# Kernel optimization log

Hardware: AMD Instinct MI355X
Metric: run time of the kernel (lower is better)

Reference implementation:

```python
import jax, jax.numpy as jnp
import numpy as np

NHEAD = 4
EPS_RMS = 1e-6
EPS_LN = 1e-5
KEEP_RATE = 0.7


def _adj_diag(num_joints=25):
    # NTU parent-child pairs; note torch.einsum('sjj,sntjc->sntjc', adj, x)
    # takes the DIAGONAL of each adjacency -> only adj_root (identity) survives,
    # adj_close/adj_far have zero diagonals. We reproduce that math faithfully.
    pairs = [(20, 1), (1, 0), (20, 2), (2, 3), (20, 4), (4, 5), (5, 6), (6, 7),
             (7, 21), (7, 22), (20, 8), (8, 9), (9, 10), (10, 11), (11, 23),
             (11, 24), (0, 12), (12, 13), (13, 14), (14, 15), (0, 16), (16, 17),
             (17, 18), (18, 19)]
    root = np.eye(num_joints, dtype=np.float32)
    close = np.zeros((num_joints, num_joints), dtype=np.float32)
    far = np.zeros((num_joints, num_joints), dtype=np.float32)
    for p, c in pairs:
        close[p, c] = 1.0
        far[c, p] = 1.0
    adj = np.stack([root, close, far])  # [3, J, J]
    return jnp.asarray(np.stack([np.diag(a) for a in adj]))  # [3, J]


def rmsnorm(x, w):
    return x * jax.lax.rsqrt(jnp.mean(x * x, -1, keepdims=True) + EPS_RMS) * w


def layernorm(x, w, b):
    m = jnp.mean(x, -1, keepdims=True)
    v = jnp.mean((x - m) ** 2, -1, keepdims=True)
    return (x - m) * jax.lax.rsqrt(v + EPS_LN) * w + b


def mha(x, in_w, in_b, out_w, out_b):
    # torch nn.MultiheadAttention (batch_first, eval: dropout off)
    B, L, C = x.shape
    H = NHEAD
    hd = C // H
    qkv = x @ in_w.T + in_b  # [B, L, 3C]
    q, k, v = jnp.split(qkv, 3, axis=-1)
    heads = lambda t: t.reshape(B, L, H, hd).transpose(0, 2, 1, 3)
    q, k, v = heads(q), heads(k), heads(v)
    attn = jax.nn.softmax(jnp.einsum('bhqd,bhkd->bhqk', q, k) / np.sqrt(hd).astype(np.float32), -1)
    o = jnp.einsum('bhqk,bhkd->bhqd', attn, v).transpose(0, 2, 1, 3).reshape(B, L, C)
    return o @ out_w.T + out_b, attn  # attn: [B, H, L, L] (average_attn_weights=False)


def reference(x, prev_spatial_attn_scores, gcn_w, g_norm_w, cls_tok, sn1_w, sn2_w,
              s_in_w, s_in_b, s_out_w, s_out_b, s_f1w, s_f1b, s_f2w, s_f2b,
              t_in_w, t_in_b, t_out_w, t_out_b, t_ln1w, t_ln1b, t_ln2w, t_ln2b,
              t_f1w, t_f1b, t_f2w, t_f2b, tn_w):
    N, T, J, _ = x.shape
    C = gcn_w.shape[-1]
    NT = N * T
    k = int(J * KEEP_RATE)
    diag = _adj_diag(J)  # [3, J]

    res = x  # residual = Identity (in_features == out_features)
    # ShiftGraphConvolution (diagonal einsum semantics) + RMSNorm
    x_gcn = rmsnorm(jnp.einsum('sj,ntjc,scd->ntjd', diag, x, gcn_w), g_norm_w)
    res_spatial = x_gcn
    xs = x_gcn.reshape(NT, J, C)

    # top-k token selection from previous cls-attention scores
    order = jnp.argsort(-prev_spatial_attn_scores, axis=1)  # descending
    idx_keep = order[:, :k]  # [NT, k]
    idx_drop = order[:, k:]  # [NT, J-k]
    ph_scores = jnp.take_along_axis(prev_spatial_attn_scores, idx_drop, 1)
    ph_norm = jax.nn.softmax(ph_scores, 1)[..., None]  # [NT, J-k, 1]
    x_inf = jnp.take_along_axis(xs, idx_keep[..., None], 1)  # [NT, k, C]
    x_ph = jnp.take_along_axis(xs, idx_drop[..., None], 1)   # [NT, J-k, C]
    x_rep = jnp.sum(x_ph * ph_norm, 1, keepdims=True)        # [NT, 1, C]

    cls = jnp.broadcast_to(cls_tok, (NT, 1, C))
    x_slow = jnp.concatenate([cls, x_inf, x_rep], 1)  # [NT, k+2, C]

    attn_out, attn_w = mha(rmsnorm(x_slow, sn1_w), s_in_w, s_in_b, s_out_w, s_out_b)
    x_msa = x_slow + attn_out
    ffn = jax.nn.gelu(rmsnorm(x_msa, sn2_w) @ s_f1w.T + s_f1b, approximate=False) @ s_f2w.T + s_f2b
    x_final_slow = x_msa + ffn

    # next spatial attention scores (cls -> other tokens, head-averaged)
    cls2others = attn_w[:, :, 0, 1:].mean(1)  # [NT, k+1]
    batch = jnp.arange(NT)[:, None]
    next_attn = jnp.zeros((NT, J), x.dtype)
    next_attn = next_attn.at[batch, idx_keep].set(cls2others[:, :k])
    next_attn = next_attn.at[batch, idx_drop].set(jnp.broadcast_to(cls2others[:, k:], (NT, J - k)))

    # scatter kept + placeholder tokens back to joint positions
    x_rep_res = attn_out[:, 1 + k:, :] + ffn[:, 1 + k:, :]  # [NT, 1, C]
    x_ph_out = x_ph + jnp.broadcast_to(x_rep_res, (NT, J - k, C))
    x_inf_out = x_final_slow[:, 1:1 + k, :]
    x_sp = jnp.zeros_like(xs)
    x_sp = x_sp.at[batch, idx_keep].set(x_inf_out)
    x_sp = x_sp.at[batch, idx_drop].set(x_ph_out)
    x_sp = x_sp.reshape(N, T, J, C) + res_spatial

    # temporal TransformerEncoderLayer (post-norm, gelu) + RMSNorm
    xt = x_sp.transpose(0, 2, 1, 3).reshape(N * J, T, C)
    a, _ = mha(xt, t_in_w, t_in_b, t_out_w, t_out_b)
    xt = layernorm(xt + a, t_ln1w, t_ln1b)
    f = jax.nn.gelu(xt @ t_f1w.T + t_f1b, approximate=False) @ t_f2w.T + t_f2b
    xt = layernorm(xt + f, t_ln2w, t_ln2b)
    xt = rmsnorm(xt, tn_w)
    x_t = xt.reshape(N, J, T, C).transpose(0, 2, 1, 3) + x_sp
    return x_t + res, next_attn


def setup_inputs() -> dict:
    key = jax.random.key(0)
    N, T, J, C, DFF = 64, 120, 25, 128, 256
    ks = jax.random.split(key, 16)
    g = lambda k_, shp: (jax.random.normal(k_, shp, jnp.float32) * 0.02)
    return {
        'x': jax.random.normal(ks[0], (N, T, J, C), jnp.float32),
        'prev_spatial_attn_scores': jax.random.uniform(ks[1], (N * T, J), jnp.float32),
        'gcn_w': g(ks[2], (3, C, C)),
        'g_norm_w': jnp.ones((C,), jnp.float32),
        'cls_tok': jnp.zeros((1, 1, C), jnp.float32),
        'sn1_w': jnp.ones((C,), jnp.float32),
        'sn2_w': jnp.ones((C,), jnp.float32),
        's_in_w': g(ks[3], (3 * C, C)), 's_in_b': jnp.zeros((3 * C,), jnp.float32),
        's_out_w': g(ks[4], (C, C)), 's_out_b': jnp.zeros((C,), jnp.float32),
        's_f1w': g(ks[5], (DFF, C)), 's_f1b': jnp.zeros((DFF,), jnp.float32),
        's_f2w': g(ks[6], (C, DFF)), 's_f2b': jnp.zeros((C,), jnp.float32),
        't_in_w': g(ks[7], (3 * C, C)), 't_in_b': jnp.zeros((3 * C,), jnp.float32),
        't_out_w': g(ks[8], (C, C)), 't_out_b': jnp.zeros((C,), jnp.float32),
        't_ln1w': jnp.ones((C,), jnp.float32), 't_ln1b': jnp.zeros((C,), jnp.float32),
        't_ln2w': jnp.ones((C,), jnp.float32), 't_ln2b': jnp.zeros((C,), jnp.float32),
        't_f1w': g(ks[9], (DFF, C)), 't_f1b': jnp.zeros((DFF,), jnp.float32),
        't_f2w': g(ks[10], (C, DFF)), 't_f2b': jnp.zeros((C,), jnp.float32),
        'tn_w': jnp.ones((C,), jnp.float32),
    }
```

## Files before the change

### kernel.cpp

```cpp
#include <hip/hip_runtime.h>
#include <hip/hip_bf16.h>
#include <math.h>

#define NTR   7680
#define NJ    25
#define NKEEP 17
#define NDRP  8
#define NL    19
#define NROW  192000
#define NTT   120
#define RSP   24

typedef __attribute__((ext_vector_type(8))) short bf16x8;
typedef __attribute__((ext_vector_type(4))) float f32x4;

__device__ __forceinline__ float gelu_exact(float v){
    return 0.5f * v * (1.0f + erff(v * 0.70710678118654752440f));
}
__device__ __forceinline__ unsigned short f2bf(float v){
    union { __hip_bfloat16 h; unsigned short u; } c;
    c.h = __float2bfloat16(v);
    return c.u;
}
__device__ __forceinline__ float bf2f(unsigned short u){
    union { unsigned u; float f; } a; a.u = ((unsigned)u) << 16; return a.f;
}

__global__ void k_prep(const float* __restrict__ s_in_w, const float* __restrict__ s_out_w,
                       const float* __restrict__ s_f1w,  const float* __restrict__ s_f2w,
                       const float* __restrict__ t_in_w, const float* __restrict__ t_out_w,
                       const float* __restrict__ t_f1w,  const float* __restrict__ t_f2w,
                       const float* __restrict__ gcnw,
                       const float* __restrict__ sn1w,   const float* __restrict__ sn2w,
                       unsigned short* __restrict__ WM)
{
    int i = blockIdx.x * 256 + threadIdx.x;
    if (i < 65536){
        const float* src;
        const float* nw = nullptr;
        int base;
        if      (i < 12288){ src = s_in_w;  base = 0;     nw = sn1w; }
        else if (i < 16384){ src = s_out_w; base = 12288; }
        else if (i < 24576){ src = s_f1w;   base = 16384; nw = sn2w; }
        else if (i < 32768){ src = s_f2w;   base = 24576; }
        else if (i < 45056){ src = t_in_w;  base = 32768; }
        else if (i < 49152){ src = t_out_w; base = 45056; }
        else if (i < 57344){ src = t_f1w;   base = 49152; }
        else               { src = t_f2w;   base = 57344; }
        int loc = i - base;
        float4 v = *(const float4*)(src + loc * 4);
        if (nw){
            float4 w = *(const float4*)(nw + ((loc * 4) & 127));
            v.x *= w.x; v.y *= w.y; v.z *= w.z; v.w *= w.w;
        }
        ushort4 o; o.x = f2bf(v.x); o.y = f2bf(v.y); o.z = f2bf(v.z); o.w = f2bf(v.w);
        *(ushort4*)(WM + i * 4) = o;
    } else if (i < 81920){
        int j = i - 65536;
        int d = j >> 7, c = j & 127;
        WM[262144 + d * 128 + c] = f2bf(gcnw[c * 128 + d]);
    }
}

__global__ __launch_bounds__(256, 3) void k_gcn_mfma(
    const float* __restrict__ x, const unsigned short* __restrict__ GWt,
    const float* __restrict__ gnw, unsigned short* __restrict__ xg)
{
    __shared__ __align__(16) unsigned short xb[64 * 136];
    __shared__ __align__(16) float yf[64 * 132];
    __shared__ float ssq[64];
    __shared__ float rstd[64];
    int tid = threadIdx.x, wv = tid >> 6, lane = tid & 63, cl = lane & 15, g = lane >> 4;
    size_t row0 = (size_t)blockIdx.x * 64;

    if (tid < 64) ssq[tid] = 0.f;
    const float4* x4 = (const float4*)(x + row0 * 128);
    for (int i = tid; i < 2048; i += 256){
        int row = i >> 5, ch = i & 31;
        float4 v = x4[row * 32 + ch];
        ushort4 o; o.x = f2bf(v.x); o.y = f2bf(v.y); o.z = f2bf(v.z); o.w = f2bf(v.w);
        *(ushort4*)(xb + row * 136 + ch * 4) = o;
    }
    __syncthreads();
    for (int job = wv; job < 32; job += 4){
        int rt = job >> 3, ct = job & 7, col = ct * 16 + cl;
        f32x4 acc = {0.f, 0.f, 0.f, 0.f};
        #pragma unroll
        for (int ks = 0; ks < 4; ks++){
            bf16x8 a = *(const bf16x8*)(xb + (rt*16 + cl)*136 + ks*32 + g*8);
            bf16x8 b = *(const bf16x8*)(GWt + col*128 + ks*32 + g*8);
            acc = __builtin_amdgcn_mfma_f32_16x16x32_bf16(a, b, acc, 0, 0, 0);
        }
        #pragma unroll
        for (int reg = 0; reg < 4; reg++){
            int row = rt*16 + g*4 + reg;
            float v = acc[reg];
            yf[row*132 + col] = v;
            float p = v * v;
            p += __shfl_xor(p, 1, 64); p += __shfl_xor(p, 2, 64);
            p += __shfl_xor(p, 4, 64); p += __shfl_xor(p, 8, 64);
            if (cl == 0) atomicAdd(&ssq[row], p);
        }
    }
    __syncthreads();
    if (tid < 64) rstd[tid] = rsqrtf(ssq[tid] * 0.0078125f + 1e-6f);
    __syncthreads();
    for (int i = tid; i < 2048; i += 256){
        int row = i >> 5, ch = i & 31;
        float4 v = *(const float4*)(yf + row*132 + ch*4);
        float4 w4 = *(const float4*)(gnw + ch*4);
        float r = rstd[row];
        ushort4 u;
        u.x = f2bf(v.x * r * w4.x); u.y = f2bf(v.y * r * w4.y);
        u.z = f2bf(v.z * r * w4.z); u.w = f2bf(v.w * r * w4.w);
        *(ushort4*)(xg + (row0 + row)*128 + ch*4) = u;
    }
}

__global__ void k_select(const float* __restrict__ sc, int* __restrict__ order,
                         int* __restrict__ slot, float* __restrict__ ph){
    int r = blockIdx.x * blockDim.x + threadIdx.x;
    if (r >= NTR) return;
    float s[NJ]; int id[NJ];
    for (int j = 0; j < NJ; j++){ s[j] = sc[r * NJ + j]; id[j] = j; }
    for (int m = 1; m < NJ; m++){
        float sv = s[m]; int iv = id[m]; int p = m;
        while (p > 0 && s[p-1] < sv){ s[p] = s[p-1]; id[p] = id[p-1]; p--; }
        s[p] = sv; id[p] = iv;
    }
    for (int j = 0; j < NJ; j++) order[r * NJ + j] = id[j];
    for (int i = 0; i < NKEEP; i++)  slot[r * NJ + id[i]] = 1 + i;
    for (int i = NKEEP; i < NJ; i++) slot[r * NJ + id[i]] = 18;
    float m8 = s[NKEEP];
    float e[NDRP]; float sum = 0.f;
    for (int i = 0; i < NDRP; i++){ e[i] = expf(s[NKEEP + i] - m8); sum += e[i]; }
    float inv = 1.f / sum;
    for (int i = 0; i < NDRP; i++) ph[r * NDRP + i] = e[i] * inv;
}

__global__ __launch_bounds__(512, 4) void k_spatial8(
    const unsigned short* __restrict__ xg, const int* __restrict__ order, const float* __restrict__ ph,
    const float* __restrict__ cls_tok,
    const unsigned short* __restrict__ WinB, const float* __restrict__ inb,
    const unsigned short* __restrict__ WoutB, const float* __restrict__ outb,
    const unsigned short* __restrict__ F1B, const float* __restrict__ f1b,
    const unsigned short* __restrict__ F2B, const float* __restrict__ f2b,
    unsigned short* __restrict__ delta, float* __restrict__ next_attn)
{
    __shared__ __align__(16) unsigned short sm[39680];
    __shared__ float rstd[48];
    __shared__ float ss2[48];
    __shared__ float clsp[8][20];
    __shared__ int   ord_s[2][NJ];
    __shared__ float ph_s[2][NDRP];
    unsigned short* xs = sm;
    unsigned short* Pb = sm + 6528;
    unsigned short* qk = sm + 16768;
    unsigned short* vT = sm + 29440;
    unsigned short* ao = sm + 29440;

    int tid = threadIdx.x;
    int r0 = blockIdx.x * 2;
    int wv = tid >> 6, lane = tid & 63, cl = lane & 15, g = lane >> 4;
    const float scale = 0.17677669529663687f;

    if (tid < 2*NJ)   ord_s[tid/NJ][tid%NJ] = order[(r0 + tid/NJ)*NJ + tid%NJ];
    if (tid < 2*NDRP) ph_s[tid>>3][tid&7]   = ph[(r0 + (tid>>3))*NDRP + (tid&7)];
    if (tid < 48) ss2[tid] = 0.f;
    for (int i = tid; i < 1280; i += 512)
        *(uint4*)(vT + i*8) = make_uint4(0,0,0,0);
    __syncthreads();

    {
        int ln = tid & 31;
        for (int j = tid >> 5; j < 48; j += 16){
            int rr = j / RSP, t = j - rr * RSP;
            const unsigned short* xgr = xg + (size_t)(r0 + rr) * NJ * 128;
            float v0, v1, v2, v3;
            if (t == 0){
                float4 cv = *(const float4*)(cls_tok + ln*4);
                v0 = cv.x; v1 = cv.y; v2 = cv.z; v3 = cv.w;
            } else if (t <= NKEEP){
                ushort4 u = *(const ushort4*)(xgr + ord_s[rr][t-1]*128 + ln*4);
                v0 = bf2f(u.x); v1 = bf2f(u.y); v2 = bf2f(u.z); v3 = bf2f(u.w);
            } else if (t == 18){
                v0 = v1 = v2 = v3 = 0.f;
                for (int i = 0; i < NDRP; i++){
                    ushort4 u = *(const ushort4*)(xgr + ord_s[rr][NKEEP+i]*128 + ln*4);
                    float w = ph_s[rr][i];
                    v0 = fmaf(bf2f(u.x),w,v0); v1 = fmaf(bf2f(u.y),w,v1);
                    v2 = fmaf(bf2f(u.z),w,v2); v3 = fmaf(bf2f(u.w),w,v3);
                }
            } else { v0 = v1 = v2 = v3 = 0.f; }
            ushort4 o4; o4.x=f2bf(v0); o4.y=f2bf(v1); o4.z=f2bf(v2); o4.w=f2bf(v3);
            *(ushort4*)(xs + j*136 + ln*4) = o4;
            float p = v0*v0 + v1*v1 + v2*v2 + v3*v3;
            p += __shfl_xor(p, 1, 64); p += __shfl_xor(p, 2, 64);
            p += __shfl_xor(p, 4, 64); p += __shfl_xor(p, 8, 64);
            p += __shfl_xor(p, 16, 64);
            if (ln == 0) rstd[j] = rsqrtf(p * 0.0078125f + 1e-6f);
        }
    }
    __syncthreads();

    {
        int col = wv*16 + cl;
        bf16x8 Bq[4], Bk[4], Bv[4];
        #pragma unroll
        for (int ks = 0; ks < 4; ks++){
            Bq[ks] = *(const bf16x8*)(WinB + col*128        + ks*32 + g*8);
            Bk[ks] = *(const bf16x8*)(WinB + (128+col)*128  + ks*32 + g*8);
            Bv[ks] = *(const bf16x8*)(WinB + (256+col)*128  + ks*32 + g*8);
        }
        float bq = inb[col], bk = inb[128+col], bv = inb[256+col];
        int h = col >> 5, d = col & 31;
        #pragma unroll
        for (int rt = 0; rt < 3; rt++){
            bf16x8 A[4];
            #pragma unroll
            for (int ks = 0; ks < 4; ks++)
                A[ks] = *(const bf16x8*)(xs + (rt*16 + cl)*136 + ks*32 + g*8);
            f32x4 aq = {0,0,0,0}, ak = {0,0,0,0}, av = {0,0,0,0};
            #pragma unroll
            for (int ks = 0; ks < 4; ks++){
                aq = __builtin_amdgcn_mfma_f32_16x16x32_bf16(A[ks], Bq[ks], aq, 0, 0, 0);
                ak = __builtin_amdgcn_mfma_f32_16x16x32_bf16(A[ks], Bk[ks], ak, 0, 0, 0);
                av = __builtin_amdgcn_mfma_f32_16x16x32_bf16(A[ks], Bv[ks], av, 0, 0, 0);
            }
            #pragma unroll
            for (int reg = 0; reg < 4; reg++){
                int row = rt*16 + g*4 + reg;
                float rs = rstd[row];
                qk[row*264 + col]       = f2bf((aq[reg]*rs + bq) * scale);
                qk[row*264 + 128 + col] = f2bf(ak[reg]*rs + bk);
                int rr = row >= RSP; int key = row - rr*RSP;
                vT[(rr*4 + h)*1280 + d*40 + key] = f2bf(av[reg]*rs + bv);
            }
        }
    }
    __syncthreads();

    {
        int qh = wv;
        int rr = qh >> 2, h = qh & 3;
        bf16x8 aq[2];
        #pragma unroll
        for (int qt = 0; qt < 2; qt++)
            aq[qt] = *(const bf16x8*)(qk + (rr*RSP + qt*16 + cl)*264 + h*32 + g*8);
        f32x4 lg[2][2];
        #pragma unroll
        for (int kt = 0; kt < 2; kt++){
            bf16x8 bk = *(const bf16x8*)(qk + (rr*RSP + kt*16 + cl)*264 + 128 + h*32 + g*8);
            f32x4 z = {0.f, 0.f, 0.f, 0.f};
            lg[0][kt] = __builtin_amdgcn_mfma_f32_16x16x32_bf16(aq[0], bk, z, 0, 0, 0);
            lg[1][kt] = __builtin_amdgcn_mfma_f32_16x16x32_bf16(aq[1], bk, z, 0, 0, 0);
        }
        #pragma unroll
        for (int qt = 0; qt < 2; qt++){
            #pragma unroll
            for (int reg = 0; reg < 4; reg++){
                float l0 = lg[qt][0][reg];
                float l1 = (cl >= 3) ? -1e30f : lg[qt][1][reg];
                float m = fmaxf(l0, l1);
                m = fmaxf(m, __shfl_xor(m, 1, 64));
                m = fmaxf(m, __shfl_xor(m, 2, 64));
                m = fmaxf(m, __shfl_xor(m, 4, 64));
                m = fmaxf(m, __shfl_xor(m, 8, 64));
                float e0 = __expf(l0 - m), e1 = __expf(l1 - m);
                float ssum = e0 + e1;
                ssum += __shfl_xor(ssum, 1, 64); ssum += __shfl_xor(ssum, 2, 64);
                ssum += __shfl_xor(ssum, 4, 64); ssum += __shfl_xor(ssum, 8, 64);
                float inv = 1.f / ssum;
                e0 *= inv; e1 *= inv;
                int q = qt*16 + g*4 + reg;
                Pb[qh*1280 + q*40 + cl]      = f2bf(e0);
                Pb[qh*1280 + q*40 + 16 + cl] = f2bf(e1);
                if (qt == 0 && g == 0 && reg == 0){
                    clsp[qh][cl] = e0;
                    if (cl < 4) clsp[qh][16 + cl] = e1;
                }
            }
        }
        bf16x8 ap[2];
        #pragma unroll
        for (int qt = 0; qt < 2; qt++)
            ap[qt] = *(const bf16x8*)(Pb + qh*1280 + (qt*16 + cl)*40 + g*8);
        #pragma unroll
        for (int dt = 0; dt < 2; dt++){
            bf16x8 bv = *(const bf16x8*)(vT + qh*1280 + (dt*16 + cl)*40 + g*8);
            #pragma unroll
            for (int qt = 0; qt < 2; qt++){
                f32x4 z = {0.f, 0.f, 0.f, 0.f};
                f32x4 oa = __builtin_amdgcn_mfma_f32_16x16x32_bf16(ap[qt], bv, z, 0, 0, 0);
                #pragma unroll
                for (int reg = 0; reg < 4; reg++){
                    int q = qt*16 + g*4 + reg;
                    if (q < 19)
                        qk[(rr*RSP + q)*264 + h*32 + dt*16 + cl] = f2bf(oa[reg]);
                    else if (q < RSP)
                        qk[(rr*RSP + q)*264 + h*32 + dt*16 + cl] = 0;
                }
            }
        }
        __syncthreads();
    }

    if (tid < 36){
        int rr2 = tid / 18, t = tid - rr2*18;
        float v = 0.25f * (clsp[rr2*4+0][1+t] + clsp[rr2*4+1][1+t] +
                           clsp[rr2*4+2][1+t] + clsp[rr2*4+3][1+t]);
        int r = r0 + rr2;
        if (t < NKEEP) next_attn[r*NJ + ord_s[rr2][t]] = v;
        else { for (int i = 0; i < NDRP; i++) next_attn[r*NJ + ord_s[rr2][NKEEP+i]] = v; }
    }

    {
        int col = wv*16 + cl;
        bf16x8 B[4];
        #pragma unroll
        for (int ks = 0; ks < 4; ks++)
            B[ks] = *(const bf16x8*)(WoutB + col*128 + ks*32 + g*8);
        float bias = outb[col];
        #pragma unroll
        for (int rt = 0; rt < 3; rt++){
            bf16x8 A[4];
            #pragma unroll
            for (int ks = 0; ks < 4; ks++)
                A[ks] = *(const bf16x8*)(qk + (rt*16 + cl)*264 + ks*32 + g*8);
            f32x4 acc = {0,0,0,0};
            #pragma unroll
            for (int ks = 0; ks < 4; ks++)
                acc = __builtin_amdgcn_mfma_f32_16x16x32_bf16(A[ks], B[ks], acc, 0, 0, 0);
            #pragma unroll
            for (int reg = 0; reg < 4; reg++){
                int row = rt*16 + g*4 + reg;
                float v = acc[reg] + bias;
                float msa = bf2f(xs[row*136 + col]) + v;
                ao[row*136 + col] = f2bf(v);
                xs[row*136 + col] = f2bf(msa);
                float p = msa * msa;
                p += __shfl_xor(p, 1, 64); p += __shfl_xor(p, 2, 64);
                p += __shfl_xor(p, 4, 64); p += __shfl_xor(p, 8, 64);
                if (cl == 0) atomicAdd(&ss2[row], p);
            }
        }
    }
    __syncthreads();

    if (tid < 48) rstd[tid] = rsqrtf(ss2[tid] * 0.0078125f + 1e-6f);
    __syncthreads();

    {
        int c0 = wv*16 + cl, c1 = c0 + 128;
        bf16x8 B0[4], B1[4];
        #pragma unroll
        for (int ks = 0; ks < 4; ks++){
            B0[ks] = *(const bf16x8*)(F1B + c0*128 + ks*32 + g*8);
            B1[ks] = *(const bf16x8*)(F1B + c1*128 + ks*32 + g*8);
        }
        float b0 = f1b[c0], b1 = f1b[c1];
        #pragma unroll
        for (int rt = 0; rt < 3; rt++){
            bf16x8 A[4];
            #pragma unroll
            for (int ks = 0; ks < 4; ks++)
                A[ks] = *(const bf16x8*)(xs + (rt*16 + cl)*136 + ks*32 + g*8);
            f32x4 a0 = {0,0,0,0}, a1 = {0,0,0,0};
            #pragma unroll
            for (int ks = 0; ks < 4; ks++){
                a0 = __builtin_amdgcn_mfma_f32_16x16x32_bf16(A[ks], B0[ks], a0, 0, 0, 0);
                a1 = __builtin_amdgcn_mfma_f32_16x16x32_bf16(A[ks], B1[ks], a1, 0, 0, 0);
            }
            #pragma unroll
            for (int reg = 0; reg < 4; reg++){
                int row = rt*16 + g*4 + reg;
                float rs = rstd[row];
                qk[row*264 + c0] = f2bf(gelu_exact(a0[reg]*rs + b0));
                qk[row*264 + c1] = f2bf(gelu_exact(a1[reg]*rs + b1));
            }
        }
    }
    __syncthreads();

    {
        int col = wv*16 + cl;
        bf16x8 B[8];
        #pragma unroll
        for (int ks = 0; ks < 8; ks++)
            B[ks] = *(const bf16x8*)(F2B + col*256 + ks*32 + g*8);
        float bias = f2b[col];
        #pragma unroll
        for (int rt = 0; rt < 3; rt++){
            bf16x8 A[8];
            #pragma unroll
            for (int ks = 0; ks < 8; ks++)
                A[ks] = *(const bf16x8*)(qk + (rt*16 + cl)*264 + ks*32 + g*8);
            f32x4 acc = {0,0,0,0};
            #pragma unroll
            for (int ks = 0; ks < 8; ks++)
                acc = __builtin_amdgcn_mfma_f32_16x16x32_bf16(A[ks], B[ks], acc, 0, 0, 0);
            #pragma unroll
            for (int reg = 0; reg < 4; reg++){
                int row = rt*16 + g*4 + reg;
                int rr = row >= RSP; int tok = row - rr*RSP;
                if (tok < 19){
                    float dv = acc[reg] + bias + bf2f(ao[row*136 + col]);
                    delta[((size_t)(r0 + rr)*19 + tok)*128 + col] = f2bf(dv);
                }
            }
        }
    }
}

__global__ void k_scatter3(const unsigned short* __restrict__ xg, const unsigned short* __restrict__ delta,
                           const int* __restrict__ slot, unsigned short* __restrict__ xb){
    int i = blockIdx.x * 256 + threadIdx.x;
    int e = i * 4;
    int c = e & 127; int rem = e >> 7;
    int t = rem % NTT; int nj = rem / NTT; int j = nj % NJ; int n = nj / NJ;
    int r = n * NTT + t;
    int sl = slot[r * NJ + j];
    ushort4 xv = *(const ushort4*)(xg + ((size_t)r * NJ + j) * 128 + c);
    ushort4 dv = *(const ushort4*)(delta + ((size_t)r * 19 + sl) * 128 + c);
    ushort4 ob;
    ob.x = f2bf(2.f * bf2f(xv.x) + bf2f(dv.x));
    ob.y = f2bf(2.f * bf2f(xv.y) + bf2f(dv.y));
    ob.z = f2bf(2.f * bf2f(xv.z) + bf2f(dv.z));
    ob.w = f2bf(2.f * bf2f(xv.w) + bf2f(dv.w));
    *(ushort4*)(xb + e) = ob;
}

__global__ __launch_bounds__(256, 3) void k_tattn2(
    const unsigned short* __restrict__ xb, const unsigned short* __restrict__ Wb,
    const float* __restrict__ inb, unsigned short* __restrict__ o)
{
    __shared__ __align__(16) unsigned short smem[22656];
    unsigned short* q_s = smem;
    unsigned short* k_s = smem + 4800;
    unsigned short* vT  = smem + 9600;
    unsigned short* P_s = smem + 13952;

    int tid = threadIdx.x;
    int l = tid & 63, cl = l & 15, g = l >> 4, wv = tid >> 6;
    int nj = blockIdx.x >> 2;
    int h  = blockIdx.x & 3;

    vT[(tid >> 3) * 136 + 120 + (tid & 7)] = 0;

    const unsigned short* xrow = xb + (size_t)nj * (NTT * 128);
    const float scale = 0.17677669529663687f;

    bf16x8 bfr[6][4];
    float bias[6];
    #pragma unroll
    for (int pc = 0; pc < 6; ++pc){
        int p = pc >> 1, s = pc & 1;
        int col = p * 128 + h * 32 + s * 16 + cl;
        bias[pc] = inb[col];
        #pragma unroll
        for (int ks = 0; ks < 4; ++ks)
            bfr[pc][ks] = *(const bf16x8*)(Wb + col * 128 + ks * 32 + g * 8);
    }

    for (int mt = wv; mt < 8; mt += 4){
        bf16x8 af[4];
        #pragma unroll
        for (int ks = 0; ks < 4; ++ks)
            af[ks] = *(const bf16x8*)(xrow + (mt * 16 + cl) * 128 + ks * 32 + g * 8);
        #pragma unroll
        for (int pc = 0; pc < 6; ++pc){
            f32x4 acc = {0.f, 0.f, 0.f, 0.f};
            #pragma unroll
            for (int ks = 0; ks < 4; ++ks)
                acc = __builtin_amdgcn_mfma_f32_16x16x32_bf16(af[ks], bfr[pc][ks], acc, 0, 0, 0);
            int p = pc >> 1, s = pc & 1;
            int d = s * 16 + cl;
            #pragma unroll
            for (int reg = 0; reg < 4; ++reg){
                int t = mt * 16 + g * 4 + reg;
                if (t < NTT){
                    float v = acc[reg] + bias[pc];
                    if (p == 0)      q_s[t * 40 + d] = f2bf(v * scale);
                    else if (p == 1) k_s[t * 40 + d] = f2bf(v);
                    else             vT[d * 136 + t] = f2bf(v);
                }
            }
        }
    }
    __syncthreads();

    for (int s = 0; s < 2; ++s){
        int mt = wv + s * 4;
        bf16x8 aq = *(const bf16x8*)(q_s + (mt * 16 + cl) * 40 + g * 8);
        f32x4 lg[8];
        #pragma unroll
        for (int jt = 0; jt < 8; ++jt){
            bf16x8 bk = *(const bf16x8*)(k_s + (jt * 16 + cl) * 40 + g * 8);
            f32x4 z = {0.f, 0.f, 0.f, 0.f};
            lg[jt] = __builtin_amdgcn_mfma_f32_16x16x32_bf16(aq, bk, z, 0, 0, 0);
        }
        if (cl >= 8){ lg[7][0] = -1e30f; lg[7][1] = -1e30f; lg[7][2] = -1e30f; lg[7][3] = -1e30f; }

        float inv[4];
        #pragma unroll
        for (int reg = 0; reg < 4; ++reg){
            float m = lg[0][reg];
            #pragma unroll
            for (int jt = 1; jt < 8; ++jt) m = fmaxf(m, lg[jt][reg]);
            m = fmaxf(m, __shfl_xor(m, 1, 64));
            m = fmaxf(m, __shfl_xor(m, 2, 64));
            m = fmaxf(m, __shfl_xor(m, 4, 64));
            m = fmaxf(m, __shfl_xor(m, 8, 64));
            float sum = 0.f;
            #pragma unroll
            for (int jt = 0; jt < 8; ++jt){ float e = __expf(lg[jt][reg] - m); lg[jt][reg] = e; sum += e; }
            sum += __shfl_xor(sum, 1, 64); sum += __shfl_xor(sum, 2, 64);
            sum += __shfl_xor(sum, 4, 64); sum += __shfl_xor(sum, 8, 64);
            inv[reg] = 1.f / sum;
        }

        unsigned short* Pw = P_s + wv * 2176;
        #pragma unroll
        for (int jt = 0; jt < 8; ++jt){
            #pragma unroll
            for (int reg = 0; reg < 4; ++reg)
                Pw[(g * 4 + reg) * 136 + jt * 16 + cl] = f2bf(lg[jt][reg] * inv[reg]);
        }

        bf16x8 ap[4];
        #pragma unroll
        for (int ks = 0; ks < 4; ++ks)
            ap[ks] = *(const bf16x8*)(Pw + cl * 136 + ks * 32 + g * 8);
        #pragma unroll
        for (int nt = 0; nt < 2; ++nt){
            f32x4 oacc = {0.f, 0.f, 0.f, 0.f};
            #pragma unroll
            for (int ks = 0; ks < 4; ++ks){
                bf16x8 bv = *(const bf16x8*)(vT + (nt * 16 + cl) * 136 + ks * 32 + g * 8);
                oacc = __builtin_amdgcn_mfma_f32_16x16x32_bf16(ap[ks], bv, oacc, 0, 0, 0);
            }
            #pragma unroll
            for (int reg = 0; reg < 4; ++reg){
                int t = mt * 16 + g * 4 + reg;
                if (t < NTT)
                    o[((size_t)nj * NTT + t) * 128 + h * 32 + nt * 16 + cl] = f2bf(oacc[reg]);
            }
        }
    }
}

__global__ __launch_bounds__(256, 4) void k_tblock(
    const unsigned short* __restrict__ o, const unsigned short* __restrict__ WoB,
    const float* __restrict__ ob, const unsigned short* __restrict__ xbres,
    const float* __restrict__ lnw, const float* __restrict__ lnb,
    const unsigned short* __restrict__ F1B, const float* __restrict__ f1b,
    const unsigned short* __restrict__ F2B, const float* __restrict__ f2b,
    const float* __restrict__ ln2w, const float* __restrict__ ln2b,
    const float* __restrict__ tnw, const float* __restrict__ x,
    float* __restrict__ out)
{
    __shared__ __align__(16) float yf[32 * 132];
    __shared__ __align__(16) unsigned short xbuf[32 * 136];
    __shared__ int xib[32];
    int tid = threadIdx.x, wv = tid >> 6, lane = tid & 63, cl = lane & 15, g = lane >> 4;
    size_t row0 = (size_t)blockIdx.x * 32;

    if (tid < 32){
        int grow = (int)row0 + tid;
        int t = grow % NTT; int njq = grow / NTT; int j = njq % NJ; int n = njq / NJ;
        xib[tid] = ((n * NTT + t) * NJ + j) * 128;
    }

    {
        int c0 = wv*16 + cl, c1 = c0 + 64;
        bf16x8 B0[4], B1[4];
        #pragma unroll
        for (int ks = 0; ks < 4; ks++){
            B0[ks] = *(const bf16x8*)(WoB + c0*128 + ks*32 + g*8);
            B1[ks] = *(const bf16x8*)(WoB + c1*128 + ks*32 + g*8);
        }
        float b0 = ob[c0], b1 = ob[c1];
        #pragma unroll
        for (int rt = 0; rt < 2; rt++){
            bf16x8 A[4];
            #pragma unroll
            for (int ks = 0; ks < 4; ks++)
                A[ks] = *(const bf16x8*)(o + (row0 + rt*16 + cl)*128 + ks*32 + g*8);
            f32x4 a0 = {0,0,0,0}, a1 = {0,0,0,0};
            #pragma unroll
            for (int ks = 0; ks < 4; ks++){
                a0 = __builtin_amdgcn_mfma_f32_16x16x32_bf16(A[ks], B0[ks], a0, 0, 0, 0);
                a1 = __builtin_amdgcn_mfma_f32_16x16x32_bf16(A[ks], B1[ks], a1, 0, 0, 0);
            }
            #pragma unroll
            for (int reg = 0; reg < 4; reg++){
                int row = rt*16 + g*4 + reg;
                yf[row*132 + c0] = a0[reg] + b0 + bf2f(xbres[(row0 + row)*128 + c0]);
                yf[row*132 + c1] = a1[reg] + b1 + bf2f(xbres[(row0 + row)*128 + c1]);
            }
        }
    }
    __syncthreads();

    {
        int row = tid >> 3, sub = tid & 7;
        float4 v[4];
        float s1 = 0.f, s2 = 0.f;
        #pragma unroll
        for (int k = 0; k < 4; k++){
            v[k] = *(const float4*)(yf + row*132 + sub*16 + k*4);
            s1 += v[k].x + v[k].y + v[k].z + v[k].w;
            s2 += v[k].x*v[k].x + v[k].y*v[k].y + v[k].z*v[k].z + v[k].w*v[k].w;
        }
        s1 += __shfl_xor(s1, 1, 64); s2 += __shfl_xor(s2, 1, 64);
        s1 += __shfl_xor(s1, 2, 64); s2 += __shfl_xor(s2, 2, 64);
        s1 += __shfl_xor(s1, 4, 64); s2 += __shfl_xor(s2, 4, 64);
        float m = s1 * 0.0078125f;
        float rv = rsqrtf(s2 * 0.0078125f - m*m + 1e-5f);
        #pragma unroll
        for (int k = 0; k < 4; k++){
            float4 w4 = *(const float4*)(lnw + sub*16 + k*4);
            float4 b4 = *(const float4*)(lnb + sub*16 + k*4);
            ushort4 u;
            u.x = f2bf((v[k].x - m) * rv * w4.x + b4.x);
            u.y = f2bf((v[k].y - m) * rv * w4.y + b4.y);
            u.z = f2bf((v[k].z - m) * rv * w4.z + b4.z);
            u.w = f2bf((v[k].w - m) * rv * w4.w + b4.w);
            *(ushort4*)(xbuf + row*136 + sub*16 + k*4) = u;
        }
    }
    __syncthreads();

    unsigned short* hb = (unsigned short*)yf;
    #pragma unroll
    for (int s = 0; s < 4; s++){
        int c = wv*16 + cl + s*64;
        bf16x8 B[4];
        #pragma unroll
        for (int ks = 0; ks < 4; ks++)
            B[ks] = *(const bf16x8*)(F1B + c*128 + ks*32 + g*8);
        float bias = f1b[c];
        #pragma unroll
        for (int rt = 0; rt < 2; rt++){
            bf16x8 A[4];
            #pragma unroll
            for (int ks = 0; ks < 4; ks++)
                A[ks] = *(const bf16x8*)(xbuf + (rt*16 + cl)*136 + ks*32 + g*8);
            f32x4 acc = {0,0,0,0};
            #pragma unroll
            for (int ks = 0; ks < 4; ks++)
                acc = __builtin_amdgcn_mfma_f32_16x16x32_bf16(A[ks], B[ks], acc, 0, 0, 0);
            #pragma unroll
            for (int reg = 0; reg < 4; reg++){
                int row = rt*16 + g*4 + reg;
                hb[row*264 + c] = f2bf(gelu_exact(acc[reg] + bias));
            }
        }
    }
    __syncthreads();

    float ys[2][2][4];
    #pragma unroll
    for (int s = 0; s < 2; s++){
        int c = wv*16 + cl + s*64;
        bf16x8 B[8];
        #pragma unroll
        for (int ks = 0; ks < 8; ks++)
            B[ks] = *(const bf16x8*)(F2B + c*256 + ks*32 + g*8);
        float bias = f2b[c];
        #pragma unroll
        for (int rt = 0; rt < 2; rt++){
            bf16x8 A[8];
            #pragma unroll
            for (int ks = 0; ks < 8; ks++)
                A[ks] = *(const bf16x8*)(hb + (rt*16 + cl)*264 + ks*32 + g*8);
            f32x4 acc = {0,0,0,0};
            #pragma unroll
            for (int ks = 0; ks < 8; ks++)
                acc = __builtin_amdgcn_mfma_f32_16x16x32_bf16(A[ks], B[ks], acc, 0, 0, 0);
            #pragma unroll
            for (int reg = 0; reg < 4; reg++){
                int row = rt*16 + g*4 + reg;
                ys[s][rt][reg] = acc[reg] + bias + bf2f(xbuf[row*136 + c]);
            }
        }
    }
    __syncthreads();
    #pragma unroll
    for (int s = 0; s < 2; s++){
        int c = wv*16 + cl + s*64;
        #pragma unroll
        for (int rt = 0; rt < 2; rt++)
            #pragma unroll
            for (int reg = 0; reg < 4; reg++)
                yf[(rt*16 + g*4 + reg)*132 + c] = ys[s][rt][reg];
    }
    __syncthreads();

    {
        int row = tid >> 3, sub = tid & 7;
        float4 v[4];
        float s1 = 0.f, s2 = 0.f;
        #pragma unroll
        for (int k = 0; k < 4; k++){
            v[k] = *(const float4*)(yf + row*132 + sub*16 + k*4);
            s1 += v[k].x + v[k].y + v[k].z + v[k].w;
            s2 += v[k].x*v[k].x + v[k].y*v[k].y + v[k].z*v[k].z + v[k].w*v[k].w;
        }
        s1 += __shfl_xor(s1, 1, 64); s2 += __shfl_xor(s2, 1, 64);
        s1 += __shfl_xor(s1, 2, 64); s2 += __shfl_xor(s2, 2, 64);
        s1 += __shfl_xor(s1, 4, 64); s2 += __shfl_xor(s2, 4, 64);
        float m = s1 * 0.0078125f;
        float rv = rsqrtf(s2 * 0.0078125f - m*m + 1e-5f);
        float z[4][4];
        float s3 = 0.f;
        #pragma unroll
        for (int k = 0; k < 4; k++){
            float4 w4 = *(const float4*)(ln2w + sub*16 + k*4);
            float4 b4 = *(const float4*)(ln2b + sub*16 + k*4);
            z[k][0] = (v[k].x - m) * rv * w4.x + b4.x;
            z[k][1] = (v[k].y - m) * rv * w4.y + b4.y;
            z[k][2] = (v[k].z - m) * rv * w4.z + b4.z;
            z[k][3] = (v[k].w - m) * rv * w4.w + b4.w;
            s3 += z[k][0]*z[k][0] + z[k][1]*z[k][1] + z[k][2]*z[k][2] + z[k][3]*z[k][3];
        }
        s3 += __shfl_xor(s3, 1, 64); s3 += __shfl_xor(s3, 2, 64); s3 += __shfl_xor(s3, 4, 64);
        float sr = rsqrtf(s3 * 0.0078125f + 1e-6f);
        int xb0 = xib[row] + sub*16;
        #pragma unroll
        for (int k = 0; k < 4; k++){
            float4 tw4 = *(const float4*)(tnw + sub*16 + k*4);
            ushort4 xr = *(const ushort4*)(xbres + (row0 + row)*128 + sub*16 + k*4);
            float4 xv = *(const float4*)(x + xb0 + k*4);
            float4 ov;
            ov.x = z[k][0] * sr * tw4.x + bf2f(xr.x) + xv.x;
            ov.y = z[k][1] * sr * tw4.y + bf2f(xr.y) + xv.y;
            ov.z = z[k][2] * sr * tw4.z + bf2f(xr.z) + xv.z;
            ov.w = z[k][3] * sr * tw4.w + bf2f(xr.w) + xv.w;
            *(float4*)(out + xb0 + k*4) = ov;
        }
    }
}

extern "C" void kernel_launch(void* const* d_in, const int* in_sizes, int n_in,
                              void* d_out, int out_size, void* d_ws, size_t ws_size,
                              hipStream_t stream) {
    (void)in_sizes; (void)n_in; (void)out_size;
    const float* x      = (const float*)d_in[0];
    const float* sc     = (const float*)d_in[1];
    const float* gcnw   = (const float*)d_in[2];
    const float* gnw    = (const float*)d_in[3];
    const float* cls    = (const float*)d_in[4];
    const float* sn1    = (const float*)d_in[5];
    const float* sn2    = (const float*)d_in[6];
    const float* s_in_w = (const float*)d_in[7];
    const float* s_in_b = (const float*)d_in[8];
    const float* s_out_w= (const float*)d_in[9];
    const float* s_out_b= (const float*)d_in[10];
    const float* s_f1w  = (const float*)d_in[11];
    const float* s_f1b  = (const float*)d_in[12];
    const float* s_f2w  = (const float*)d_in[13];
    const float* s_f2b  = (const float*)d_in[14];
    const float* t_in_w = (const float*)d_in[15];
    const float* t_in_b = (const float*)d_in[16];
    const float* t_out_w= (const float*)d_in[17];
    const float* t_out_b= (const float*)d_in[18];
    const float* t_ln1w = (const float*)d_in[19];
    const float* t_ln1b = (const float*)d_in[20];
    const float* t_ln2w = (const float*)d_in[21];
    const float* t_ln2b = (const float*)d_in[22];
    const float* t_f1w  = (const float*)d_in[23];
    const float* t_f1b  = (const float*)d_in[24];
    const float* t_f2w  = (const float*)d_in[25];
    const float* t_f2b  = (const float*)d_in[26];
    const float* tnw    = (const float*)d_in[27];

    char* ws = (char*)d_ws;
    const size_t SZ_BIG = 98304000;
    char*  R1 = ws;
    char*  R2 = ws + SZ_BIG;
    char*  R3 = ws + 2 * SZ_BIG;
    char* p = ws + 3 * SZ_BIG;
    int*   ORD  = (int*)p;   p += 768000;
    int*   SLOT = (int*)p;   p += 768000;
    float* PH   = (float*)p; p += 245760;
    unsigned short* WM = (unsigned short*)p; p += 557056;
    if (ws_size < (size_t)(p - ws)) return;

    unsigned short* WinB  = WM;
    unsigned short* WoutB = WM + 49152;
    unsigned short* F1B   = WM + 65536;
    unsigned short* F2B   = WM + 98304;
    unsigned short* WB    = WM + 131072;
    unsigned short* WoBt  = WM + 180224;
    unsigned short* F1Bt  = WM + 196608;
    unsigned short* F2Bt  = WM + 229376;
    unsigned short* GWt   = WM + 262144;

    unsigned short* XG  = (unsigned short*)R1;
    unsigned short* DLT = (unsigned short*)R3;
    unsigned short* XB  = (unsigned short*)(R3 + 37355520);
    unsigned short* OB  = (unsigned short*)R2;

    float* out0 = (float*)d_out;
    float* next_attn = out0 + 24576000;

    k_prep<<<320, 256, 0, stream>>>(s_in_w, s_out_w, s_f1w, s_f2w,
                                    t_in_w, t_out_w, t_f1w, t_f2w, gcnw,
                                    sn1, sn2, WM);
    k_gcn_mfma<<<3000, 256, 0, stream>>>(x, GWt, gnw, XG);
    k_select<<<30, 256, 0, stream>>>(sc, ORD, SLOT, PH);
    k_spatial8<<<3840, 512, 0, stream>>>(XG, ORD, PH, cls,
                                         WinB, s_in_b, WoutB, s_out_b,
                                         F1B, s_f1b, F2B, s_f2b,
                                         DLT, next_attn);
    k_scatter3<<<24000, 256, 0, stream>>>(XG, DLT, SLOT, XB);
    k_tattn2<<<6400, 256, 0, stream>>>(XB, WB, t_in_b, OB);
    k_tblock<<<6000, 256, 0, stream>>>(OB, WoBt, t_out_b, XB,
                                       t_ln1w, t_ln1b, F1Bt, t_f1b,
                                       F2Bt, t_f2b, t_ln2w, t_ln2b,
                                       tnw, x, out0);
}
```

Baseline: 654.1 us.

## Fuse GCN projection and RMSNorm into spatial attention kernel

Removes the standalone GCN MFMA kernel and computes the per-joint GCN matmul plus RMSNorm inside the spatial kernel for each pair of frames, keeping the normalized result in shared memory for token gathering. The kernel still writes XG to global memory for the later scatter stage. This saves one launch and the global re-read of XG by the spatial kernel. In exchange, the spatial kernel takes on extra shared-memory staging, more syncs and more register pressure. It also pads 50 rows to 64, which wastes some MFMA work.

After: 630.6 us. 1.04x faster.

```diff
diff --git a/kernel.cpp b/kernel.cpp
--- a/kernel.cpp
+++ b/kernel.cpp
@@ -62,61 +62,6 @@
     }
 }
 
-__global__ __launch_bounds__(256, 3) void k_gcn_mfma(
-    const float* __restrict__ x, const unsigned short* __restrict__ GWt,
-    const float* __restrict__ gnw, unsigned short* __restrict__ xg)
-{
-    __shared__ __align__(16) unsigned short xb[64 * 136];
-    __shared__ __align__(16) float yf[64 * 132];
-    __shared__ float ssq[64];
-    __shared__ float rstd[64];
-    int tid = threadIdx.x, wv = tid >> 6, lane = tid & 63, cl = lane & 15, g = lane >> 4;
-    size_t row0 = (size_t)blockIdx.x * 64;
-
-    if (tid < 64) ssq[tid] = 0.f;
-    const float4* x4 = (const float4*)(x + row0 * 128);
-    for (int i = tid; i < 2048; i += 256){
-        int row = i >> 5, ch = i & 31;
-        float4 v = x4[row * 32 + ch];
-        ushort4 o; o.x = f2bf(v.x); o.y = f2bf(v.y); o.z = f2bf(v.z); o.w = f2bf(v.w);
-        *(ushort4*)(xb + row * 136 + ch * 4) = o;
-    }
-    __syncthreads();
-    for (int job = wv; job < 32; job += 4){
-        int rt = job >> 3, ct = job & 7, col = ct * 16 + cl;
-        f32x4 acc = {0.f, 0.f, 0.f, 0.f};
-        #pragma unroll
-        for (int ks = 0; ks < 4; ks++){
-            bf16x8 a = *(const bf16x8*)(xb + (rt*16 + cl)*136 + ks*32 + g*8);
-            bf16x8 b = *(const bf16x8*)(GWt + col*128 + ks*32 + g*8);
-            acc = __builtin_amdgcn_mfma_f32_16x16x32_bf16(a, b, acc, 0, 0, 0);
-        }
-        #pragma unroll
-        for (int reg = 0; reg < 4; reg++){
-            int row = rt*16 + g*4 + reg;
-            float v = acc[reg];
-            yf[row*132 + col] = v;
-            float p = v * v;
-            p += __shfl_xor(p, 1, 64); p += __shfl_xor(p, 2, 64);
-            p += __shfl_xor(p, 4, 64); p += __shfl_xor(p, 8, 64);
-            if (cl == 0) atomicAdd(&ssq[row], p);
-        }
-    }
-    __syncthreads();
-    if (tid < 64) rstd[tid] = rsqrtf(ssq[tid] * 0.0078125f + 1e-6f);
-    __syncthreads();
-    for (int i = tid; i < 2048; i += 256){
-        int row = i >> 5, ch = i & 31;
-        float4 v = *(const float4*)(yf + row*132 + ch*4);
-        float4 w4 = *(const float4*)(gnw + ch*4);
-        float r = rstd[row];
-        ushort4 u;
-        u.x = f2bf(v.x * r * w4.x); u.y = f2bf(v.y * r * w4.y);
-        u.z = f2bf(v.z * r * w4.z); u.w = f2bf(v.w * r * w4.w);
-        *(ushort4*)(xg + (row0 + row)*128 + ch*4) = u;
-    }
-}
-
 __global__ void k_select(const float* __restrict__ sc, int* __restrict__ order,
                          int* __restrict__ slot, float* __restrict__ ph){
     int r = blockIdx.x * blockDim.x + threadIdx.x;
@@ -138,13 +83,15 @@
     for (int i = 0; i < NDRP; i++) ph[r * NDRP + i] = e[i] * inv;
 }
 
-__global__ __launch_bounds__(512, 4) void k_spatial8(
-    const unsigned short* __restrict__ xg, const int* __restrict__ order, const float* __restrict__ ph,
+__global__ __launch_bounds__(512, 4) void k_spatial9(
+    const float* __restrict__ x, const unsigned short* __restrict__ GWt, const float* __restrict__ gnw,
+    const int* __restrict__ order, const float* __restrict__ ph,
     const float* __restrict__ cls_tok,
     const unsigned short* __restrict__ WinB, const float* __restrict__ inb,
     const unsigned short* __restrict__ WoutB, const float* __restrict__ outb,
     const unsigned short* __restrict__ F1B, const float* __restrict__ f1b,
     const unsigned short* __restrict__ F2B, const float* __restrict__ f2b,
+    unsigned short* __restrict__ xg_out,
     unsigned short* __restrict__ delta, float* __restrict__ next_attn)
 {
     __shared__ __align__(16) unsigned short sm[39680];
@@ -153,11 +100,14 @@
     __shared__ float clsp[8][20];
     __shared__ int   ord_s[2][NJ];
     __shared__ float ph_s[2][NDRP];
-    unsigned short* xs = sm;
-    unsigned short* Pb = sm + 6528;
-    unsigned short* qk = sm + 16768;
-    unsigned short* vT = sm + 29440;
-    unsigned short* ao = sm + 29440;
+    unsigned short* xs     = sm;
+    unsigned short* xstage = sm + 6528;
+    unsigned short* Pb     = sm + 6528;
+    unsigned short* xgl    = sm + 16768;
+    unsigned short* qk     = sm + 16768;
+    unsigned short* vT     = sm + 29440;
+    unsigned short* ao     = sm + 29440;
+    float* gss = &clsp[0][0];
 
     int tid = threadIdx.x;
     int r0 = blockIdx.x * 2;
@@ -167,26 +117,94 @@
     if (tid < 2*NJ)   ord_s[tid/NJ][tid%NJ] = order[(r0 + tid/NJ)*NJ + tid%NJ];
     if (tid < 2*NDRP) ph_s[tid>>3][tid&7]   = ph[(r0 + (tid>>3))*NDRP + (tid&7)];
     if (tid < 48) ss2[tid] = 0.f;
+    if (tid < 64) gss[tid] = 0.f;
     for (int i = tid; i < 1280; i += 512)
         *(uint4*)(vT + i*8) = make_uint4(0,0,0,0);
-    __syncthreads();
+
+    {
+        const float* xr = x + (size_t)r0 * NJ * 128;
+        for (int i = tid; i < 2048; i += 512){
+            int row = i >> 5, ch = i & 31;
+            ushort4 u;
+            if (row < 50){
+                float4 v = *(const float4*)(xr + row*128 + ch*4);
+                u.x = f2bf(v.x); u.y = f2bf(v.y); u.z = f2bf(v.z); u.w = f2bf(v.w);
+            } else { u.x = 0; u.y = 0; u.z = 0; u.w = 0; }
+            *(ushort4*)(xstage + row*136 + ch*4) = u;
+        }
+    }
+    __syncthreads();
+
+    f32x4 gacc[4];
+    {
+        int col = wv*16 + cl;
+        bf16x8 Bg[4];
+        #pragma unroll
+        for (int ks = 0; ks < 4; ks++)
+            Bg[ks] = *(const bf16x8*)(GWt + col*128 + ks*32 + g*8);
+        #pragma unroll
+        for (int rt = 0; rt < 4; rt++){
+            bf16x8 A[4];
+            #pragma unroll
+            for (int ks = 0; ks < 4; ks++)
+                A[ks] = *(const bf16x8*)(xstage + (rt*16 + cl)*136 + ks*32 + g*8);
+            f32x4 acc = {0,0,0,0};
+            #pragma unroll
+            for (int ks = 0; ks < 4; ks++)
+                acc = __builtin_amdgcn_mfma_f32_16x16x32_bf16(A[ks], Bg[ks], acc, 0, 0, 0);
+            gacc[rt] = acc;
+            #pragma unroll
+            for (int reg = 0; reg < 4; reg++){
+                int row = rt*16 + g*4 + reg;
+                float p = acc[reg] * acc[reg];
+                p += __shfl_xor(p, 1, 64); p += __shfl_xor(p, 2, 64);
+                p += __shfl_xor(p, 4, 64); p += __shfl_xor(p, 8, 64);
+                if (cl == 0) atomicAdd(&gss[row], p);
+            }
+        }
+    }
+    __syncthreads();
+    if (tid < 64) gss[tid] = rsqrtf(gss[tid] * 0.0078125f + 1e-6f);
+    __syncthreads();
+    {
+        int col = wv*16 + cl;
+        float gw = gnw[col];
+        #pragma unroll
+        for (int rt = 0; rt < 4; rt++){
+            #pragma unroll
+            for (int reg = 0; reg < 4; reg++){
+                int row = rt*16 + g*4 + reg;
+                if (row < 50)
+                    xgl[row*136 + col] = f2bf(gacc[rt][reg] * gss[row] * gw);
+            }
+        }
+    }
+    __syncthreads();
+
+    {
+        unsigned short* dst = xg_out + (size_t)r0 * NJ * 128;
+        for (int i = tid; i < 1600; i += 512){
+            int row = i >> 5, ch = i & 31;
+            *(ushort4*)(dst + row*128 + ch*4) = *(const ushort4*)(xgl + row*136 + ch*4);
+        }
+    }
 
     {
         int ln = tid & 31;
         for (int j = tid >> 5; j < 48; j += 16){
             int rr = j / RSP, t = j - rr * RSP;
-            const unsigned short* xgr = xg + (size_t)(r0 + rr) * NJ * 128;
+            const unsigned short* xgr = xgl + rr * NJ * 136;
             float v0, v1, v2, v3;
             if (t == 0){
                 float4 cv = *(const float4*)(cls_tok + ln*4);
                 v0 = cv.x; v1 = cv.y; v2 = cv.z; v3 = cv.w;
             } else if (t <= NKEEP){
-                ushort4 u = *(const ushort4*)(xgr + ord_s[rr][t-1]*128 + ln*4);
+                ushort4 u = *(const ushort4*)(xgr + ord_s[rr][t-1]*136 + ln*4);
                 v0 = bf2f(u.x); v1 = bf2f(u.y); v2 = bf2f(u.z); v3 = bf2f(u.w);
             } else if (t == 18){
                 v0 = v1 = v2 = v3 = 0.f;
                 for (int i = 0; i < NDRP; i++){
-                    ushort4 u = *(const ushort4*)(xgr + ord_s[rr][NKEEP+i]*128 + ln*4);
+                    ushort4 u = *(const ushort4*)(xgr + ord_s[rr][NKEEP+i]*136 + ln*4);
                     float w = ph_s[rr][i];
                     v0 = fmaf(bf2f(u.x),w,v0); v1 = fmaf(bf2f(u.y),w,v1);
                     v2 = fmaf(bf2f(u.z),w,v2); v3 = fmaf(bf2f(u.w),w,v3);
@@ -808,12 +826,11 @@
     k_prep<<<320, 256, 0, stream>>>(s_in_w, s_out_w, s_f1w, s_f2w,
                                     t_in_w, t_out_w, t_f1w, t_f2w, gcnw,
                                     sn1, sn2, WM);
-    k_gcn_mfma<<<3000, 256, 0, stream>>>(x, GWt, gnw, XG);
     k_select<<<30, 256, 0, stream>>>(sc, ORD, SLOT, PH);
-    k_spatial8<<<3840, 512, 0, stream>>>(XG, ORD, PH, cls,
+    k_spatial9<<<3840, 512, 0, stream>>>(x, GWt, gnw, ORD, PH, cls,
                                          WinB, s_in_b, WoutB, s_out_b,
                                          F1B, s_f1b, F2B, s_f2b,
-                                         DLT, next_attn);
+                                         XG, DLT, next_attn);
     k_scatter3<<<24000, 256, 0, stream>>>(XG, DLT, SLOT, XB);
     k_tattn2<<<6400, 256, 0, stream>>>(XB, WB, t_in_b, OB);
     k_tblock<<<6000, 256, 0, stream>>>(OB, WoBt, t_out_b, XB,
```
